# Performance work log

Hardware: AMD Instinct MI355X
Metric: run time of the kernel (lower is better)

Reference implementation:

```python
import jax, jax.numpy as jnp
import numpy as np

N_NODES = 50000
N_EDGES = 800000
F_IN = 128
C = 64
NODE_DEG = 32  # edges forced to touch node 0


def setup_inputs() -> dict:
    key = jax.random.key(0)
    ks = jax.random.split(key, 10)
    x = jax.random.normal(ks[0], (N_NODES, F_IN), dtype=jnp.float32)
    # random edges over nodes 1..N-1, then force the first NODE_DEG edges to have src == 0
    src = jax.random.randint(ks[1], (N_EDGES,), 1, N_NODES)
    dst = jax.random.randint(ks[2], (N_EDGES,), 1, N_NODES)
    src = src.at[:NODE_DEG].set(0)
    edge_index = jnp.stack([src, dst]).astype(jnp.int64)
    pos = jax.random.normal(ks[3], (N_NODES, 2), dtype=jnp.float32)
    batch = jnp.zeros((N_NODES,), dtype=jnp.int64)
    s1 = 1.0 / np.sqrt(F_IN)
    s2 = 1.0 / np.sqrt(C)
    w1 = jax.random.uniform(ks[4], (F_IN, C), jnp.float32, -s1, s1)
    b1 = jnp.zeros((C,), jnp.float32)
    w2 = jax.random.uniform(ks[5], (C, C), jnp.float32, -s2, s2)
    b2 = jnp.zeros((C,), jnp.float32)
    w_ro = jax.random.uniform(ks[6], (C, 1), jnp.float32, -s2, s2)
    b_ro = jnp.zeros((1,), jnp.float32)
    return {"x": x, "edge_index": edge_index, "pos": pos, "node": 0,
            "batch": batch, "w1": w1, "b1": b1, "w2": w2, "b2": b2,
            "w_ro": w_ro, "b_ro": b_ro}


def gcn_conv(x, src, dst, w, b, n_nodes):
    # PyG GCNConv: linear -> symmetric normalization with self-loops -> scatter-add
    xw = x @ w  # [N, C]
    deg = jax.ops.segment_sum(jnp.ones_like(dst, dtype=xw.dtype), dst,
                              num_segments=n_nodes) + 1.0  # +1 self-loop
    dinv = jax.lax.rsqrt(deg)
    norm = dinv[src] * dinv[dst]  # [E]
    agg = jax.ops.segment_sum(norm[:, None] * xw[src], dst, num_segments=n_nodes)
    agg = agg + xw * (dinv * dinv)[:, None]  # self-loop contribution
    return agg + b


def reference(x, edge_index, pos, node, batch, w1, b1, w2, b2, w_ro, b_ro):
    n_nodes = x.shape[0]
    src, dst = edge_index[0], edge_index[1]
    h = jax.nn.relu(gcn_conv(x, src, dst, w1, b1, n_nodes))
    h = jax.nn.relu(gcn_conv(h, src, dst, w2, b2, n_nodes))
    # select edges incident to `node` (data-dependent size; eager boolean indexing)
    mask = (src == node) | (dst == node)
    rel = edge_index[:, mask]  # [2, K]
    targets = jnp.where(rel[0] == node, rel[1], rel[0])  # [K]
    score = jax.nn.sigmoid(h[targets] @ w_ro + b_ro)  # [K, 1]
    return score[:, 0], targets
```

## Files before the change

kernel.cpp:

```cpp
#include <hip/hip_runtime.h>
#include <math.h>

#define F_IN 128
#define C 64
#define ELCAP 128
#define E2CAP 4096
#define E1CAP 32768
#define S1CAP 4096
#define NBW 1568
#define SCAP 512
#define NSCAN 256

#define I_EL 0
#define I_E2 1
#define I_E1 2
#define I_S1 3

__global__ __launch_bounds__(256) void mask_kernel(const int* __restrict__ src,
    const int* __restrict__ dst, const int* __restrict__ node_p,
    unsigned* __restrict__ tbits, unsigned* __restrict__ s1bits,
    int* __restrict__ map1, int* __restrict__ elist, int* __restrict__ s1list,
    int* __restrict__ e1s, int* __restrict__ e1d, int* __restrict__ cnt, int nq) {
  int q = blockIdx.x * 256 + threadIdx.x;
  if (q >= nq) return;
  int node = *node_p;
  int4 s4 = ((const int4*)src)[q];
  int4 d4 = ((const int4*)dst)[q];
  int ss[4] = {s4.x, s4.y, s4.z, s4.w};
  int dd[4] = {d4.x, d4.y, d4.z, d4.w};
#pragma unroll
  for (int j = 0; j < 4; ++j) {
    int s = ss[j], d = dd[j];
    if (s == node || d == node) {
      int p = atomicAdd(&cnt[I_EL], 1);
      if (p < ELCAP) elist[p] = q * 4 + j;
      int tgt = (s == node) ? d : s;
      atomicOr(&tbits[tgt >> 5], 1u << (tgt & 31));
      unsigned old = atomicOr(&s1bits[tgt >> 5], 1u << (tgt & 31));
      if (!((old >> (tgt & 31)) & 1)) {
        int idx = atomicAdd(&cnt[I_S1], 1);
        if (idx < S1CAP) { s1list[idx] = tgt; map1[tgt] = idx; }
        int pe = atomicAdd(&cnt[I_E1], 1);
        if (pe < E1CAP) { e1s[pe] = tgt; e1d[pe] = tgt; }
      }
    }
  }
}

__global__ __launch_bounds__(256) void scanB_kernel(const int* __restrict__ src,
    const int* __restrict__ dst, const unsigned* __restrict__ tbits,
    unsigned* __restrict__ s1bits, int* __restrict__ map1, int* __restrict__ s1list,
    int* __restrict__ e2s, int* __restrict__ e2d, int* __restrict__ e1s,
    int* __restrict__ e1d, int* __restrict__ cnt, int nq) {
  __shared__ unsigned tb[NBW];
  __shared__ int ebS[SCAP], ebD[SCAP], nb[SCAP];
  __shared__ int cA, cB, bA, bB, bC;
  int t = threadIdx.x;
  for (int i = t; i < NBW; i += 256) tb[i] = tbits[i];
  if (t == 0) { cA = 0; cB = 0; }
  __syncthreads();
  const int4* s4p = (const int4*)src;
  const int4* d4p = (const int4*)dst;
  for (int q = blockIdx.x * 256 + t; q < nq; q += gridDim.x * 256) {
    int4 d4 = d4p[q];
    int4 s4 = s4p[q];
    int dd[4] = {d4.x, d4.y, d4.z, d4.w};
    int ss[4] = {s4.x, s4.y, s4.z, s4.w};
#pragma unroll
    for (int j = 0; j < 4; ++j) {
      int d = dd[j];
      if ((tb[d >> 5] >> (d & 31)) & 1) {
        int s = ss[j];
        int p = atomicAdd(&cA, 1);
        if (p < SCAP) { ebS[p] = s; ebD[p] = d; }
        else { int g = atomicAdd(&cnt[I_E2], 1); if (g < E2CAP) { e2s[g] = s; e2d[g] = d; } }
        unsigned old = atomicOr(&s1bits[s >> 5], 1u << (s & 31));
        if (!((old >> (s & 31)) & 1)) {
          int p2 = atomicAdd(&cB, 1);
          if (p2 < SCAP) nb[p2] = s;
          else {
            int idx = atomicAdd(&cnt[I_S1], 1);
            if (idx < S1CAP) { s1list[idx] = s; map1[s] = idx; }
            int pe = atomicAdd(&cnt[I_E1], 1);
            if (pe < E1CAP) { e1s[pe] = s; e1d[pe] = s; }
          }
        }
      }
    }
  }
  __syncthreads();
  int nA = min(cA, SCAP), nB = min(cB, SCAP);
  if (t == 0) {
    bA = atomicAdd(&cnt[I_E2], nA);
    bB = atomicAdd(&cnt[I_S1], nB);
    bC = atomicAdd(&cnt[I_E1], nB);
  }
  __syncthreads();
  for (int i = t; i < nA; i += 256) {
    int g = bA + i; if (g < E2CAP) { e2s[g] = ebS[i]; e2d[g] = ebD[i]; }
  }
  for (int i = t; i < nB; i += 256) {
    int v = nb[i];
    int idx = bB + i; if (idx < S1CAP) { s1list[idx] = v; map1[v] = idx; }
    int pe = bC + i; if (pe < E1CAP) { e1s[pe] = v; e1d[pe] = v; }
  }
}

__global__ __launch_bounds__(256) void scanC_kernel(const int* __restrict__ src,
    const int* __restrict__ dst, const unsigned* __restrict__ s1bits,
    unsigned* __restrict__ s0bits, int* __restrict__ e1s, int* __restrict__ e1d,
    int* __restrict__ cnt, int nq) {
  __shared__ unsigned sb[NBW];
  __shared__ int ebS[SCAP], ebD[SCAP];
  __shared__ int cA, bA;
  int t = threadIdx.x;
  for (int i = t; i < NBW; i += 256) sb[i] = s1bits[i];
  if (t == 0) cA = 0;
  __syncthreads();
  const int4* s4p = (const int4*)src;
  const int4* d4p = (const int4*)dst;
  for (int q = blockIdx.x * 256 + t; q < nq; q += gridDim.x * 256) {
    int4 d4 = d4p[q];
    int4 s4 = s4p[q];
    int dd[4] = {d4.x, d4.y, d4.z, d4.w};
    int ss[4] = {s4.x, s4.y, s4.z, s4.w};
#pragma unroll
    for (int j = 0; j < 4; ++j) {
      int d = dd[j];
      if ((sb[d >> 5] >> (d & 31)) & 1) {
        int s = ss[j];
        atomicOr(&s0bits[s >> 5], 1u << (s & 31));
        int p = atomicAdd(&cA, 1);
        if (p < SCAP) { ebS[p] = s; ebD[p] = d; }
        else { int g = atomicAdd(&cnt[I_E1], 1); if (g < E1CAP) { e1s[g] = s; e1d[g] = d; } }
      }
    }
  }
  __syncthreads();
  int nA = min(cA, SCAP);
  if (t == 0) bA = atomicAdd(&cnt[I_E1], nA);
  __syncthreads();
  for (int i = t; i < nA; i += 256) {
    int g = bA + i; if (g < E1CAP) { e1s[g] = ebS[i]; e1d[g] = ebD[i]; }
  }
}

__global__ __launch_bounds__(256) void deg_kernel(const int* __restrict__ dst,
    const unsigned* __restrict__ s0bits, const unsigned* __restrict__ s1bits,
    int* __restrict__ deg, int nq) {
  __shared__ unsigned cb[NBW];
  int t = threadIdx.x;
  for (int i = t; i < NBW; i += 256) cb[i] = s0bits[i] | s1bits[i];
  __syncthreads();
  const int4* d4p = (const int4*)dst;
  for (int q = blockIdx.x * 256 + t; q < nq; q += gridDim.x * 256) {
    int4 d4 = d4p[q];
    int dd[4] = {d4.x, d4.y, d4.z, d4.w};
#pragma unroll
    for (int j = 0; j < 4; ++j) {
      int d = dd[j];
      if ((cb[d >> 5] >> (d & 31)) & 1) atomicAdd(&deg[d], 1);
    }
  }
}

__global__ __launch_bounds__(256) void edgegemm1_kernel(const float* __restrict__ x,
    const float* __restrict__ w, const int* __restrict__ e1s,
    const int* __restrict__ e1d, const int* __restrict__ deg,
    const int* __restrict__ map1, float* __restrict__ agg1c,
    const int* __restrict__ cnt) {
  __shared__ float ws[F_IN * C];
  __shared__ float xs[32 * F_IN];
  __shared__ int qidx[32];
  __shared__ float wgt[32];
  int t = threadIdx.x;
  int n1 = cnt[I_E1]; if (n1 > E1CAP) n1 = E1CAP;
  int s1c = cnt[I_S1]; if (s1c > S1CAP) s1c = S1CAP;
  int ntile = (n1 + 31) / 32;
  if ((int)blockIdx.x >= ntile) return;
  for (int i = t; i < F_IN * C; i += 256) ws[i] = w[i];
  for (int tile = blockIdx.x; tile < ntile; tile += gridDim.x) {
    __syncthreads();
    int r0 = tile * 32;
    for (int i = t; i < 32 * F_IN; i += 256) {
      int r = r0 + (i >> 7);
      xs[i] = (r < n1) ? x[(size_t)e1s[r] * F_IN + (i & 127)] : 0.0f;
    }
    if (t < 32) {
      int r = r0 + t;
      if (r < n1) {
        int s = e1s[r], d = e1d[r];
        int q = map1[d];
        qidx[t] = ((unsigned)q < (unsigned)s1c) ? q : -1;
        wgt[t] = rsqrtf((float)deg[s] + 1.0f) * rsqrtf((float)deg[d] + 1.0f);
      } else qidx[t] = -1;
    }
    __syncthreads();
    int c = t & 63, rb = t >> 6;
    float acc[8];
#pragma unroll
    for (int j = 0; j < 8; ++j) acc[j] = 0.f;
    for (int k = 0; k < F_IN; ++k) {
      float wv = ws[k * C + c];
#pragma unroll
      for (int j = 0; j < 8; ++j)
        acc[j] += xs[(rb + j * 4) * F_IN + k] * wv;
    }
#pragma unroll
    for (int j = 0; j < 8; ++j) {
      int r = rb + j * 4;
      int q = qidx[r];
      if (q >= 0) atomicAdd(&agg1c[(size_t)q * C + c], acc[j] * wgt[r]);
    }
  }
}

__global__ __launch_bounds__(256) void gemm2c_kernel(const float* __restrict__ agg1c,
    const float* __restrict__ b1, const float* __restrict__ w,
    float* __restrict__ xw2c, const int* __restrict__ cnt) {
  __shared__ float ws[C * C];
  __shared__ float xs[64 * C];
  int t = threadIdx.x;
  int sc = cnt[I_S1]; if (sc > S1CAP) sc = S1CAP;
  for (int i = t; i < C * C; i += 256) ws[i] = w[i];
  int ntile = (sc + 63) / 64;
  for (int tile = blockIdx.x; tile < ntile; tile += gridDim.x) {
    __syncthreads();
    int r0 = tile * 64;
    for (int i = t; i < 64 * C; i += 256) {
      int r = r0 + (i >> 6), cc = i & 63;
      xs[i] = (r < sc) ? fmaxf(agg1c[(size_t)r * C + cc] + b1[cc], 0.0f) : 0.0f;
    }
    __syncthreads();
    int c = t & 63, rb = t >> 6;
    float acc[16];
#pragma unroll
    for (int j = 0; j < 16; ++j) acc[j] = 0.f;
    for (int k = 0; k < C; ++k) {
      float wv = ws[k * C + c];
#pragma unroll
      for (int j = 0; j < 16; ++j)
        acc[j] += xs[(rb + j * 4) * C + k] * wv;
    }
#pragma unroll
    for (int j = 0; j < 16; ++j) {
      int r = r0 + rb + j * 4;
      if (r < sc) xw2c[(size_t)r * C + c] = acc[j];
    }
  }
}

__global__ __launch_bounds__(256) void gather2_kernel(const int* __restrict__ e2s,
    const int* __restrict__ e2d, const int* __restrict__ deg,
    const int* __restrict__ map1, const float* __restrict__ xw2c,
    float* __restrict__ agg2c, const int* __restrict__ cnt) {
  int n2 = cnt[I_E2]; if (n2 > E2CAP) n2 = E2CAP;
  int gid = blockIdx.x * 256 + threadIdx.x;
  int i = gid >> 6, lane = gid & 63;
  int stride = (gridDim.x * 256) >> 6;
  for (; i < n2; i += stride) {
    int s = e2s[i], d = e2d[i];
    int q = map1[d];
    if ((unsigned)q < (unsigned)ELCAP) {
      float w = rsqrtf((float)deg[s] + 1.0f) * rsqrtf((float)deg[d] + 1.0f);
      atomicAdd(&agg2c[(size_t)q * C + lane], w * xw2c[(size_t)map1[s] * C + lane]);
    }
  }
}

__global__ __launch_bounds__(1024) void readout_kernel(const int* __restrict__ src,
    const int* __restrict__ dst, const float* __restrict__ agg2c,
    const int* __restrict__ deg, const int* __restrict__ map1,
    const float* __restrict__ xw2c, const float* __restrict__ b2,
    const float* __restrict__ w_ro, const float* __restrict__ b_ro,
    const int* __restrict__ node_p, const int* __restrict__ elist,
    const int* __restrict__ cnt, int K, float* __restrict__ out) {
  __shared__ int ids[ELCAP];
  __shared__ float wro_s[C], b2_s[C];
  int t = threadIdx.x;
  int n = cnt[I_EL];
  if (n > K) n = K;
  if (n > ELCAP) n = ELCAP;
  if (t < C) { wro_s[t] = w_ro[t]; b2_s[t] = b2[t]; }
  for (int i = t; i < n; i += 1024) ids[i] = elist[i];
  __syncthreads();
  int node = *node_p;
  float bro = b_ro[0];
  int wid = t >> 6, lane = t & 63;
  for (int i = wid; i < n; i += 16) {
    int eid = ids[i];
    int rank = 0;
    for (int j = 0; j < n; ++j) rank += (ids[j] < eid) ? 1 : 0;
    int s = src[eid], d = dst[eid];
    int tgt = (s == node) ? d : s;
    int q = map1[tgt];
    float dv = rsqrtf((float)deg[tgt] + 1.0f);
    float h = agg2c[(size_t)q * C + lane] + xw2c[(size_t)q * C + lane] * dv * dv
            + b2_s[lane];
    float v = fmaxf(h, 0.0f) * wro_s[lane];
#pragma unroll
    for (int off = 1; off < 64; off <<= 1) v += __shfl_xor(v, off, 64);
    if (lane == 0) {
      float acc = v + bro;
      out[rank] = 1.0f / (1.0f + expf(-acc));
      out[K + rank] = (float)tgt;
    }
  }
}

extern "C" void kernel_launch(void* const* d_in, const int* in_sizes, int n_in,
                              void* d_out, int out_size, void* d_ws, size_t ws_size,
                              hipStream_t stream) {
  const float* x    = (const float*)d_in[0];
  const int*   ei   = (const int*)d_in[1];
  const int*   node = (const int*)d_in[3];
  const float* w1   = (const float*)d_in[5];
  const float* b1   = (const float*)d_in[6];
  const float* w2   = (const float*)d_in[7];
  const float* b2   = (const float*)d_in[8];
  const float* w_ro = (const float*)d_in[9];
  const float* b_ro = (const float*)d_in[10];
  float* out = (float*)d_out;

  int nE = in_sizes[1] / 2;
  int nN = in_sizes[0] / F_IN;
  const int* src = ei;
  const int* dst = ei + nE;
  int K = out_size / 2;
  int nq = nE / 4;

  int* w = (int*)d_ws;
  int*      deg    = w;            w += nN;
  unsigned* tbits  = (unsigned*)w; w += NBW;
  unsigned* s1bits = (unsigned*)w; w += NBW;
  unsigned* s0bits = (unsigned*)w; w += NBW;
  int*      cnt    = w;            w += 16;
  float*    agg1c  = (float*)w;    w += (size_t)S1CAP * C;
  float*    agg2c  = (float*)w;    w += (size_t)ELCAP * C;
  int*      map1   = w;            w += nN;
  int*      elist  = w;            w += ELCAP;
  int*      s1list = w;            w += S1CAP;
  int*      e2s    = w;            w += E2CAP;
  int*      e2d    = w;            w += E2CAP;
  int*      e1s    = w;            w += E1CAP;
  int*      e1d    = w;            w += E1CAP;
  float*    xw2c   = (float*)w;    w += (size_t)S1CAP * C;

  hipMemsetAsync(deg, 0,
      ((size_t)nN + 3 * NBW + 16 + (size_t)S1CAP * C + (size_t)ELCAP * C) * 4, stream);

  mask_kernel<<<(nq + 255) / 256, 256, 0, stream>>>(src, dst, node, tbits, s1bits,
      map1, elist, s1list, e1s, e1d, cnt, nq);
  scanB_kernel<<<NSCAN, 256, 0, stream>>>(src, dst, tbits, s1bits, map1, s1list,
      e2s, e2d, e1s, e1d, cnt, nq);
  scanC_kernel<<<NSCAN, 256, 0, stream>>>(src, dst, s1bits, s0bits, e1s, e1d, cnt, nq);
  deg_kernel<<<NSCAN, 256, 0, stream>>>(dst, s0bits, s1bits, deg, nq);
  edgegemm1_kernel<<<512, 256, 0, stream>>>(x, w1, e1s, e1d, deg, map1, agg1c, cnt);
  gemm2c_kernel<<<16, 256, 0, stream>>>(agg1c, b1, w2, xw2c, cnt);
  gather2_kernel<<<64, 256, 0, stream>>>(e2s, e2d, deg, map1, xw2c, agg2c, cnt);
  readout_kernel<<<1, 1024, 0, stream>>>(src, dst, agg2c, deg, map1, xw2c, b2,
                                         w_ro, b_ro, node, elist, cnt, K, out);
}
```

Baseline: 88.00 us.

## Fuse gather2 and readout via last-block atomic counter; load src lazily in scans

Merges the gather2 and readout kernels into one launch. The last block to finish, detected through an atomic done-counter with thread fences, performs the readout. Both scan kernels now read src only for edges whose dst bit matches instead of vector-loading all of it, which cuts scan bandwidth roughly in half. The scan grid is doubled. Risks: the readout now runs with 256 threads instead of 1024, the lazy src loads are uncoalesced, and the done-counter relies on cnt[I_DONE] being covered by the memset.

```diff
diff --git a/kernel.cpp b/kernel.cpp
--- a/kernel.cpp
+++ b/kernel.cpp
@@ -9,12 +9,14 @@
 #define S1CAP 4096
 #define NBW 1568
 #define SCAP 512
-#define NSCAN 256
+#define NSCAN 512
+#define NG2 64
 
 #define I_EL 0
 #define I_E2 1
 #define I_E1 2
 #define I_S1 3
+#define I_DONE 4
 
 __global__ __launch_bounds__(256) void mask_kernel(const int* __restrict__ src,
     const int* __restrict__ dst, const int* __restrict__ node_p,
@@ -59,18 +61,15 @@
   for (int i = t; i < NBW; i += 256) tb[i] = tbits[i];
   if (t == 0) { cA = 0; cB = 0; }
   __syncthreads();
-  const int4* s4p = (const int4*)src;
   const int4* d4p = (const int4*)dst;
   for (int q = blockIdx.x * 256 + t; q < nq; q += gridDim.x * 256) {
     int4 d4 = d4p[q];
-    int4 s4 = s4p[q];
     int dd[4] = {d4.x, d4.y, d4.z, d4.w};
-    int ss[4] = {s4.x, s4.y, s4.z, s4.w};
 #pragma unroll
     for (int j = 0; j < 4; ++j) {
       int d = dd[j];
       if ((tb[d >> 5] >> (d & 31)) & 1) {
-        int s = ss[j];
+        int s = src[q * 4 + j];
         int p = atomicAdd(&cA, 1);
         if (p < SCAP) { ebS[p] = s; ebD[p] = d; }
         else { int g = atomicAdd(&cnt[I_E2], 1); if (g < E2CAP) { e2s[g] = s; e2d[g] = d; } }
@@ -117,18 +116,15 @@
   for (int i = t; i < NBW; i += 256) sb[i] = s1bits[i];
   if (t == 0) cA = 0;
   __syncthreads();
-  const int4* s4p = (const int4*)src;
   const int4* d4p = (const int4*)dst;
   for (int q = blockIdx.x * 256 + t; q < nq; q += gridDim.x * 256) {
     int4 d4 = d4p[q];
-    int4 s4 = s4p[q];
     int dd[4] = {d4.x, d4.y, d4.z, d4.w};
-    int ss[4] = {s4.x, s4.y, s4.z, s4.w};
 #pragma unroll
     for (int j = 0; j < 4; ++j) {
       int d = dd[j];
       if ((sb[d >> 5] >> (d & 31)) & 1) {
-        int s = ss[j];
+        int s = src[q * 4 + j];
         atomicOr(&s0bits[s >> 5], 1u << (s & 31));
         int p = atomicAdd(&cA, 1);
         if (p < SCAP) { ebS[p] = s; ebD[p] = d; }
@@ -250,44 +246,53 @@
   }
 }
 
-__global__ __launch_bounds__(256) void gather2_kernel(const int* __restrict__ e2s,
+__global__ __launch_bounds__(256) void gather2_kernel(const int* __restrict__ src,
+    const int* __restrict__ dst, const int* __restrict__ e2s,
     const int* __restrict__ e2d, const int* __restrict__ deg,
     const int* __restrict__ map1, const float* __restrict__ xw2c,
-    float* __restrict__ agg2c, const int* __restrict__ cnt) {
-  int n2 = cnt[I_E2]; if (n2 > E2CAP) n2 = E2CAP;
-  int gid = blockIdx.x * 256 + threadIdx.x;
-  int i = gid >> 6, lane = gid & 63;
-  int stride = (gridDim.x * 256) >> 6;
-  for (; i < n2; i += stride) {
-    int s = e2s[i], d = e2d[i];
-    int q = map1[d];
-    if ((unsigned)q < (unsigned)ELCAP) {
-      float w = rsqrtf((float)deg[s] + 1.0f) * rsqrtf((float)deg[d] + 1.0f);
-      atomicAdd(&agg2c[(size_t)q * C + lane], w * xw2c[(size_t)map1[s] * C + lane]);
-    }
-  }
-}
-
-__global__ __launch_bounds__(1024) void readout_kernel(const int* __restrict__ src,
-    const int* __restrict__ dst, const float* __restrict__ agg2c,
-    const int* __restrict__ deg, const int* __restrict__ map1,
-    const float* __restrict__ xw2c, const float* __restrict__ b2,
+    float* __restrict__ agg2c, const float* __restrict__ b2,
     const float* __restrict__ w_ro, const float* __restrict__ b_ro,
     const int* __restrict__ node_p, const int* __restrict__ elist,
-    const int* __restrict__ cnt, int K, float* __restrict__ out) {
+    int* __restrict__ cnt, int K, float* __restrict__ out) {
+  int t = threadIdx.x;
+  {
+    int n2 = cnt[I_E2]; if (n2 > E2CAP) n2 = E2CAP;
+    int gid = blockIdx.x * 256 + t;
+    int i = gid >> 6, lane = gid & 63;
+    int stride = (NG2 * 256) >> 6;
+    for (; i < n2; i += stride) {
+      int s = e2s[i], d = e2d[i];
+      int q = map1[d];
+      if ((unsigned)q < (unsigned)ELCAP) {
+        float w = rsqrtf((float)deg[s] + 1.0f) * rsqrtf((float)deg[d] + 1.0f);
+        atomicAdd(&agg2c[(size_t)q * C + lane], w * xw2c[(size_t)map1[s] * C + lane]);
+      }
+    }
+  }
+  __shared__ int lastFlag;
+  __syncthreads();
+  if (t == 0) {
+    __threadfence();
+    int done = atomicAdd(&cnt[I_DONE], 1);
+    lastFlag = (done == NG2 - 1);
+  }
+  __syncthreads();
+  if (!lastFlag) return;
+  if (t == 0) __threadfence();
+  __syncthreads();
+
   __shared__ int ids[ELCAP];
   __shared__ float wro_s[C], b2_s[C];
-  int t = threadIdx.x;
   int n = cnt[I_EL];
   if (n > K) n = K;
   if (n > ELCAP) n = ELCAP;
   if (t < C) { wro_s[t] = w_ro[t]; b2_s[t] = b2[t]; }
-  for (int i = t; i < n; i += 1024) ids[i] = elist[i];
+  for (int i = t; i < n; i += 256) ids[i] = elist[i];
   __syncthreads();
   int node = *node_p;
   float bro = b_ro[0];
   int wid = t >> 6, lane = t & 63;
-  for (int i = wid; i < n; i += 16) {
+  for (int i = wid; i < n; i += 4) {
     int eid = ids[i];
     int rank = 0;
     for (int j = 0; j < n; ++j) rank += (ids[j] < eid) ? 1 : 0;
@@ -357,7 +362,6 @@
   deg_kernel<<<NSCAN, 256, 0, stream>>>(dst, s0bits, s1bits, deg, nq);
   edgegemm1_kernel<<<512, 256, 0, stream>>>(x, w1, e1s, e1d, deg, map1, agg1c, cnt);
   gemm2c_kernel<<<16, 256, 0, stream>>>(agg1c, b1, w2, xw2c, cnt);
-  gather2_kernel<<<64, 256, 0, stream>>>(e2s, e2d, deg, map1, xw2c, agg2c, cnt);
-  readout_kernel<<<1, 1024, 0, stream>>>(src, dst, agg2c, deg, map1, xw2c, b2,
-                                         w_ro, b_ro, node, elist, cnt, K, out);
-}
+  gather2_kernel<<<NG2, 256, 0, stream>>>(src, dst, e2s, e2d, deg, map1, xw2c,
+      agg2c, b2, w_ro, b_ro, node, elist, cnt, K, out);
+}
```

New measurement: 103.8 us. 17.9% more time.
